# Kernel optimization log

Hardware: AMD Instinct MI355X
Metric: run time of the kernel (lower is better)

Reference implementation:

```python
import jax, jax.numpy as jnp
import numpy as np

N_NODES = 50000
N_EDGES = 500000
D_NODE = 256
D_EDGE = 256
FINAL_OUT = 256
NEG_SLOPE = 0.01  # torch LeakyReLU default


def _linear_params(key, d_in, d_out):
    kw, kb = jax.random.split(key)
    s = 1.0 / np.sqrt(d_in)
    W = jax.random.uniform(kw, (d_in, d_out), jnp.float32, -s, s)
    b = jax.random.uniform(kb, (d_out,), jnp.float32, -s, s)
    return W, b


def setup_inputs() -> dict:
    key = jax.random.key(0)
    ks = jax.random.split(key, 8)
    in1 = D_NODE + D_EDGE          # 512
    hid1 = 2 * in1                 # 1024
    out1 = hid1 // 2               # 512
    in2 = out1 + D_NODE            # 768
    hid2 = 2 * in2                 # 1536
    W1, b1 = _linear_params(ks[0], in1, hid1)
    W2, b2 = _linear_params(ks[1], hid1, out1)
    W3, b3 = _linear_params(ks[2], in2, hid2)
    W4, b4 = _linear_params(ks[3], hid2, FINAL_OUT)
    x = jax.random.normal(ks[4], (N_NODES, D_NODE), jnp.float32)
    edge_attr = jax.random.normal(ks[5], (N_EDGES, D_EDGE), jnp.float32)
    edge_index = jax.random.randint(ks[6], (2, N_EDGES), 0, N_NODES, jnp.int64)
    u = jax.random.normal(ks[7], (1, 16), jnp.float32)
    batch = jnp.zeros((N_NODES,), jnp.int64)
    return {"x": x, "edge_index": edge_index, "edge_attr": edge_attr,
            "u": u, "batch": batch,
            "W1": W1, "b1": b1, "W2": W2, "b2": b2,
            "W3": W3, "b3": b3, "W4": W4, "b4": b4}


def _leaky(v):
    return jnp.where(v >= 0, v, NEG_SLOPE * v)


def reference(x, edge_index, edge_attr, u, batch, W1, b1, W2, b2, W3, b3, W4, b4):
    row, col = edge_index[0], edge_index[1]
    # gather source-node features and concat edge features: [E, D_NODE+D_EDGE]
    m = jnp.concatenate([x[row], edge_attr], axis=1)
    # node_mlp_1
    m = _leaky(m @ W1 + b1) @ W2 + b2            # [E, out1]
    # scatter-mean over destination nodes (count clamped to 1, as torch_scatter)
    agg = jax.ops.segment_sum(m, col, num_segments=x.shape[0])
    cnt = jax.ops.segment_sum(jnp.ones((m.shape[0],), m.dtype), col,
                              num_segments=x.shape[0])
    agg = agg / jnp.maximum(cnt, 1.0)[:, None]   # [N, out1]
    # node_mlp_2
    h = jnp.concatenate([x, agg], axis=1)        # [N, in2]
    return _leaky(h @ W3 + b3) @ W4 + b4         # [N, FINAL_OUT]
```

## Files before the change

### kernel.cpp

```cpp
#include <hip/hip_runtime.h>

typedef __bf16 bf16x8 __attribute__((ext_vector_type(8)));
typedef float fx4 __attribute__((ext_vector_type(4)));
typedef unsigned short u16x8 __attribute__((ext_vector_type(8)));
typedef unsigned short u16x4 __attribute__((ext_vector_type(4)));

__device__ __forceinline__ unsigned short f2b(float f) {
  unsigned u = __float_as_uint(f);
  u = (u + 0x7fffu + ((u >> 16) & 1u)) >> 16;
  return (unsigned short)u;
}
__device__ __forceinline__ float b2f(unsigned short s) {
  return __uint_as_float((unsigned)s << 16);
}

__device__ __forceinline__ void gload16(const void* g, void* l) {
  __builtin_amdgcn_global_load_lds(
      (const __attribute__((address_space(1))) unsigned int*)g,
      (__attribute__((address_space(3))) unsigned int*)l, 16, 0, 0);
}

template<int MODE, int K, int N, int NT, bool EAB>
__global__ __launch_bounds__(256)
void gemm_k(const unsigned short* __restrict__ A,
            const unsigned short* __restrict__ xb,
            const unsigned short* __restrict__ eas,
            const float* __restrict__ eaf,
            const float* __restrict__ aggH_in,
            const float* __restrict__ cnt,
            const unsigned short* __restrict__ agg2b_in,
            const unsigned short* __restrict__ zxb,
            const int* __restrict__ perm,
            const int* __restrict__ ssrc,
            const int* __restrict__ sdst,
            const unsigned short* __restrict__ Bt,
            const float* __restrict__ bias,
            float* __restrict__ outf,
            unsigned short* __restrict__ outb,
            int M, int base, int mt, int mtc)
{
  const int bid = blockIdx.x;
  const int xcd = bid & 7;
  const int sl  = bid >> 3;
  const int tile_n = sl % NT;
  const int tile_m = xcd * mtc + sl / NT;
  if (tile_m >= mt) return;
  const int mbase = tile_m * 128;

  constexpr int SMEM = (MODE == 1) ? 51216 : 16384;
  __shared__ __align__(16) char smem[SMEM];
  unsigned short* Al = (unsigned short*)smem;
  unsigned short* Bl = (unsigned short*)(smem + 8192);

  const int t = threadIdx.x;
  const int w = t >> 6, l = t & 63;
  const int wr = w >> 1, wc = w & 1;
  const int lr = l & 15, lk = l >> 4;

  fx4 zero = {0.f, 0.f, 0.f, 0.f};
  fx4 acc[4][4];
#pragma unroll
  for (int i = 0; i < 4; i++)
#pragma unroll
    for (int j = 0; j < 4; j++) acc[i][j] = zero;

  if constexpr (MODE == 1) {
#pragma unroll
    for (int q = 0; q < 8; ++q) {
      const int c = q * 256 + t;
      const int zrow = c >> 4, zu = c & 15;
      int gr = mbase + zrow; if (gr >= M) gr = M - 1;
      gload16(zxb + (size_t)ssrc[gr] * 1024 + tile_n * 128 + zu * 8,
              (char*)smem + 18448 + c * 16);
    }
  }

  for (int k0 = 0; k0 < K; k0 += 32) {
#pragma unroll
    for (int it = 0; it < 2; ++it) {
      const int c = t + it * 256;
      const int row = c >> 2, u = c & 3;
      gload16(Bt + (size_t)(tile_n * 128 + row) * K + (k0 + u * 8),
              (char*)Bl + c * 16);
      int rl = mbase + row; if (rl >= M) rl = M - 1;
      if constexpr (MODE == 1) {
        if constexpr (EAB) {
          gload16(eas + (size_t)rl * 256 + (k0 + u * 8), (char*)Al + c * 16);
        } else {
          const int e = perm[rl];
          const float* s = eaf + (size_t)e * 256 + (k0 + u * 8);
          fx4 f0 = *(const fx4*)s, f1 = *(const fx4*)(s + 4);
          u16x8 v;
          v[0]=f2b(f0[0]); v[1]=f2b(f0[1]); v[2]=f2b(f0[2]); v[3]=f2b(f0[3]);
          v[4]=f2b(f1[0]); v[5]=f2b(f1[1]); v[6]=f2b(f1[2]); v[7]=f2b(f1[3]);
          *(u16x8*)((char*)Al + c * 16) = v;
        }
      } else if constexpr (MODE == 2) {
        const float ct = cnt[rl];
        const float rs = 1.f / fmaxf(ct, 1.f);
        const float* s = aggH_in + (size_t)rl * 1024 + (k0 + u * 8);
        fx4 f0 = *(const fx4*)s, f1 = *(const fx4*)(s + 4);
        u16x8 v;
        v[0]=f2b(f0[0]*rs); v[1]=f2b(f0[1]*rs); v[2]=f2b(f0[2]*rs); v[3]=f2b(f0[3]*rs);
        v[4]=f2b(f1[0]*rs); v[5]=f2b(f1[1]*rs); v[6]=f2b(f1[2]*rs); v[7]=f2b(f1[3]*rs);
        *(u16x8*)((char*)Al + c * 16) = v;
      } else if constexpr (MODE == 3) {
        const int node = base + rl;
        if (k0 < 256)
          gload16(xb + (size_t)node * 256 + (k0 + u * 8), (char*)Al + c * 16);
        else
          gload16(agg2b_in + (size_t)node * 512 + (k0 - 256) + u * 8,
                  (char*)Al + c * 16);
      } else if constexpr (MODE == 5) {
        gload16(xb + (size_t)rl * 256 + (k0 + u * 8), (char*)Al + c * 16);
      } else {
        gload16(A + (size_t)rl * K + (k0 + u * 8), (char*)Al + c * 16);
      }
    }
    __syncthreads();

    bf16x8 af[4], bfr[4];
    const int mb0 = wr * 64, nb0 = wc * 64;
#pragma unroll
    for (int i = 0; i < 4; i++)
      af[i] = *(const bf16x8*)(Al + (mb0 + i * 16 + lr) * 32 + lk * 8);
#pragma unroll
    for (int j = 0; j < 4; j++)
      bfr[j] = *(const bf16x8*)(Bl + (nb0 + j * 16 + lr) * 32 + lk * 8);
#pragma unroll
    for (int i = 0; i < 4; i++)
#pragma unroll
      for (int j = 0; j < 4; j++)
        acc[i][j] = __builtin_amdgcn_mfma_f32_16x16x32_bf16(af[i], bfr[j],
                                                            acc[i][j], 0, 0, 0);
    __syncthreads();
  }

  if constexpr (MODE == 1) {
    int rows = M - mbase; if (rows > 128) rows = 128;
    unsigned short* CL = (unsigned short*)smem;
    int* runs_s = (int*)(smem + 16896);
    int* runs_e = (int*)(smem + 17408);
    int* runs_d = (int*)(smem + 17920);
    unsigned long long* wmask = (unsigned long long*)(smem + 18432);
    const unsigned short* ZL = (const unsigned short*)(smem + 18448);
    int flag = 0;
    if (t < 128)
      flag = (t < rows) && ((t == 0) || (sdst[mbase + t] != sdst[mbase + t - 1]));
    unsigned long long bm = __ballot(flag);
    if (l == 0 && w < 2) wmask[w] = bm;
    __syncthreads();
    const unsigned long long m0 = wmask[0], m1 = wmask[1];
    const int nruns = __builtin_popcountll(m0) + __builtin_popcountll(m1);
    if (flag) {
      int rank, rend;
      if (t < 64) {
        rank = __builtin_popcountll(m0 & ((t == 0) ? 0ull : ((1ull << t) - 1)));
        unsigned long long above = (t == 63) ? 0ull : (m0 & (~0ull << (t + 1)));
        if (above) rend = __builtin_ctzll(above);
        else if (m1) rend = 64 + __builtin_ctzll(m1);
        else rend = rows;
      } else {
        const int tt = t - 64;
        rank = __builtin_popcountll(m0) +
               __builtin_popcountll(m1 & ((tt == 0) ? 0ull : ((1ull << tt) - 1)));
        unsigned long long above = (tt == 63) ? 0ull : (m1 & (~0ull << (tt + 1)));
        rend = above ? 64 + __builtin_ctzll(above) : rows;
      }
      runs_s[rank] = t; runs_e[rank] = rend; runs_d[rank] = sdst[mbase + t];
    }
    const int lc = wc * 16 + lr;
    const int nn_base = tile_n * 128 + wc * 64 + lr;
    for (int jj = 0; jj < 2; ++jj) {
#pragma unroll
      for (int jp = 0; jp < 2; ++jp) {
        const int j = jj * 2 + jp;
        const float bj = bias[nn_base + j * 16];
        const int cloc = wc * 64 + j * 16 + lr;
#pragma unroll
        for (int i = 0; i < 4; i++)
#pragma unroll
          for (int r = 0; r < 4; r++) {
            const int lrow = wr * 64 + i * 16 + lk * 4 + r;
            float v = acc[i][j][r] + bj + b2f(ZL[lrow * 128 + cloc]);
            v = v >= 0.f ? v : 0.01f * v;
            CL[lrow * 66 + jp * 32 + lc] = f2b(v);
          }
      }
      __syncthreads();
      for (int task = t; task < nruns * 64; task += 256) {
        const int ri = task >> 6, c = task & 63;
        const int rs = runs_s[ri], re = runs_e[ri];
        float s = 0.f;
        for (int r = rs; r < re; ++r) s += b2f(CL[r * 66 + c]);
        const int jp = c >> 5, w16 = (c >> 4) & 1, clr = c & 15;
        const int n = tile_n * 128 + w16 * 64 + (jj * 2 + jp) * 16 + clr;
        float* addr = outf + (size_t)runs_d[ri] * 1024 + n;
        const bool open = (rs == 0 && mbase > 0) || (re == rows && mbase + rows < M);
        if (open) atomicAdd(addr, s); else *addr = s;
      }
      __syncthreads();
    }
  } else {
#pragma unroll
    for (int j = 0; j < 4; j++) {
      const int n = tile_n * 128 + wc * 64 + j * 16 + lr;
      float bj = 0.f;
      if constexpr (MODE == 2 || MODE == 3 || MODE == 4) bj = bias[n];
#pragma unroll
      for (int i = 0; i < 4; i++) {
        const int m0 = mbase + wr * 64 + i * 16 + lk * 4;
#pragma unroll
        for (int r = 0; r < 4; r++) {
          const int m = m0 + r;
          if (m < M) {
            float v = acc[i][j][r];
            if constexpr (MODE == 2) {
              v += (cnt[m] > 0.f ? bj : 0.f);
              outb[(size_t)m * N + n] = f2b(v);
            } else if constexpr (MODE == 3) {
              v += bj;
              v = v >= 0.f ? v : 0.01f * v;
              outb[(size_t)m * N + n] = f2b(v);
            } else if constexpr (MODE == 5) {
              outb[(size_t)m * N + n] = f2b(v);
            } else {
              outf[(size_t)(base + m) * N + n] = v + bj;
            }
          }
        }
      }
    }
  }
}

__global__ void fix_idx_k(const int* __restrict__ src, int* __restrict__ dst, int n2) {
  int i = blockIdx.x * blockDim.x + threadIdx.x;
  if (i >= n2) return;
  bool is64 = true;
#pragma unroll
  for (int p = 0; p < 16; ++p) is64 = is64 && (src[2 * p + 1] == 0);
  dst[i] = is64 ? src[2 * i] : src[i];
}

__global__ void cvt_f2b_k(const float* __restrict__ x, unsigned short* __restrict__ o,
                          long n4) {
  long i = (long)blockIdx.x * blockDim.x + threadIdx.x;
  if (i < n4) {
    fx4 f = *(const fx4*)(x + i * 4);
    u16x4 v; v[0]=f2b(f[0]); v[1]=f2b(f[1]); v[2]=f2b(f[2]); v[3]=f2b(f[3]);
    *(u16x4*)(o + i * 4) = v;
  }
}

__global__ void cvt_eas_k(const float* __restrict__ ea, const int* __restrict__ perm,
                          unsigned short* __restrict__ eas, int E) {
  long i = (long)blockIdx.x * blockDim.x + threadIdx.x;
  if (i >= (long)E * 64) return;
  const int s = (int)(i >> 6), q = (int)(i & 63);
  const float* src = ea + (size_t)perm[s] * 256 + q * 4;
  fx4 f = *(const fx4*)src;
  u16x4 v; v[0]=f2b(f[0]); v[1]=f2b(f[1]); v[2]=f2b(f[2]); v[3]=f2b(f[3]);
  *(u16x4*)(eas + (size_t)s * 256 + q * 4) = v;
}

__global__ void cvt_w_k(const float* __restrict__ W, unsigned short* __restrict__ Wt,
                        int K, int N) {
  long i = (long)blockIdx.x * blockDim.x + threadIdx.x;
  if (i < (long)K * N) {
    int k = (int)(i / N), n = (int)(i % N);
    Wt[(size_t)n * K + k] = f2b(W[i]);
  }
}

__global__ void cnt_kk(const int* __restrict__ ecol, float* __restrict__ cnt, int E) {
  int i = blockIdx.x * blockDim.x + threadIdx.x;
  if (i < E) atomicAdd(cnt + ecol[i], 1.f);
}

__global__ __launch_bounds__(1024)
void scan_k(const float* __restrict__ cnt, int* __restrict__ pos, int Nn) {
  __shared__ int sdata[1024];
  __shared__ int carry;
  if (threadIdx.x == 0) carry = 0;
  __syncthreads();
  for (int bb = 0; bb < Nn; bb += 1024) {
    const int i = bb + threadIdx.x;
    const int v = (i < Nn) ? (int)cnt[i] : 0;
    sdata[threadIdx.x] = v;
    __syncthreads();
    for (int off = 1; off < 1024; off <<= 1) {
      int tv = (threadIdx.x >= off) ? sdata[threadIdx.x - off] : 0;
      __syncthreads();
      sdata[threadIdx.x] += tv;
      __syncthreads();
    }
    const int excl = sdata[threadIdx.x] - v + carry;
    if (i < Nn) pos[i] = excl;
    __syncthreads();
    if (threadIdx.x == 1023) carry += sdata[1023];
    __syncthreads();
  }
}

__global__ void perm_k(const int* __restrict__ idx, int E, int* __restrict__ pos,
                       int* __restrict__ perm, int* __restrict__ ssrc,
                       int* __restrict__ sdst) {
  int e = blockIdx.x * blockDim.x + threadIdx.x;
  if (e >= E) return;
  const int d = idx[E + e];
  const int s = atomicAdd(pos + d, 1);
  perm[s] = e;
  ssrc[s] = idx[e];
  sdst[s] = d;
}

extern "C" void kernel_launch(void* const* d_in, const int* in_sizes, int n_in,
                              void* d_out, int out_size, void* d_ws, size_t ws_size,
                              hipStream_t stream)
{
  const float* x  = (const float*)d_in[0];
  const int* eraw = (const int*)d_in[1];
  const float* ea = (const float*)d_in[2];
  const float* W1 = (const float*)d_in[5];
  const float* b1 = (const float*)d_in[6];
  const float* W2 = (const float*)d_in[7];
  const float* b2 = (const float*)d_in[8];
  const float* W3 = (const float*)d_in[9];
  const float* b3 = (const float*)d_in[10];
  const float* W4 = (const float*)d_in[11];
  const float* b4 = (const float*)d_in[12];
  float* out = (float*)d_out;

  const int Nn = in_sizes[0] / 256;
  const int E  = in_sizes[1] / 2;

  char* p = (char*)d_ws;
  auto take = [&](size_t bytes) -> char* {
    char* r = p; p += (bytes + 255) & ~(size_t)255; return r;
  };
  unsigned short* W1xt = (unsigned short*)take((size_t)1024 * 256 * 2);
  unsigned short* W1et = (unsigned short*)take((size_t)1024 * 256 * 2);
  unsigned short* W2t  = (unsigned short*)take((size_t)1024 * 512 * 2);
  unsigned short* W3t  = (unsigned short*)take((size_t)768 * 1536 * 2);
  unsigned short* W4t  = (unsigned short*)take((size_t)1536 * 256 * 2);
  int* idx  = (int*)take((size_t)2 * E * 4);
  float* cnt  = (float*)take((size_t)Nn * 4);
  float* aggH = (float*)take((size_t)Nn * 1024 * 4);
  size_t zlen = (size_t)(p - (char*)cnt);
  unsigned short* agg2b = (unsigned short*)take((size_t)Nn * 512 * 2);
  unsigned short* xb    = (unsigned short*)take((size_t)Nn * 256 * 2);
  unsigned short* zxb   = (unsigned short*)take((size_t)Nn * 1024 * 2);
  int* pos  = (int*)take((size_t)Nn * 4);
  int* perm = (int*)take((size_t)E * 4);
  int* ssrc = (int*)take((size_t)E * 4);
  int* sdst = (int*)take((size_t)E * 4);

  long avail = (long)ws_size - (long)(p - (char*)d_ws);

  unsigned short* eas = nullptr;
  const long eas_bytes = (((long)E * 256 * 2) + 255) & ~255L;
  if (avail >= eas_bytes + 128 * 3072 + 1024) {
    eas = (unsigned short*)take((size_t)E * 256 * 2);
    avail -= eas_bytes;
  }
  long bandN = avail / 3072;  bandN &= ~127L;
  if (bandN > 50048) bandN = 50048;
  if (bandN < 128)   bandN = 128;
  unsigned short* H3 = (unsigned short*)take((size_t)bandN * 3072);

  hipMemsetAsync(cnt, 0, zlen, stream);
  fix_idx_k<<<(2 * E + 255) / 256, 256, 0, stream>>>(eraw, idx, 2 * E);
  cnt_kk<<<(E + 255) / 256, 256, 0, stream>>>(idx + E, cnt, E);
  scan_k<<<1, 1024, 0, stream>>>(cnt, pos, Nn);
  perm_k<<<(E + 255) / 256, 256, 0, stream>>>(idx, E, pos, perm, ssrc, sdst);
  cvt_f2b_k<<<(Nn * 64 + 255) / 256, 256, 0, stream>>>(x, xb, (long)Nn * 64);
  if (eas)
    cvt_eas_k<<<(int)(((long)E * 64 + 255) / 256), 256, 0, stream>>>(ea, perm,
                                                                     eas, E);
  cvt_w_k<<<(256 * 1024 + 255) / 256, 256, 0, stream>>>(W1, W1xt, 256, 1024);
  cvt_w_k<<<(256 * 1024 + 255) / 256, 256, 0, stream>>>(W1 + 256 * 1024, W1et,
                                                        256, 1024);
  cvt_w_k<<<(1024 * 512 + 255) / 256, 256, 0, stream>>>(W2, W2t, 1024, 512);
  cvt_w_k<<<(768 * 1536 + 255) / 256, 256, 0, stream>>>(W3, W3t, 768, 1536);
  cvt_w_k<<<(1536 * 256 + 255) / 256, 256, 0, stream>>>(W4, W4t, 1536, 256);

  {
    const int mt = (Nn + 127) / 128, mtc = (mt + 7) / 8;
    gemm_k<5, 256, 1024, 8, false><<<mtc * 8 * 8, 256, 0, stream>>>(
        nullptr, xb, nullptr, nullptr, nullptr, nullptr, nullptr, nullptr,
        nullptr, nullptr, nullptr, W1xt, nullptr, nullptr, zxb, Nn, 0, mt, mtc);
  }

  {
    const int mt = (E + 127) / 128, mtc = (mt + 7) / 8;
    const int grid = mtc * 8 * 8;
    if (eas)
      gemm_k<1, 256, 1024, 8, true><<<grid, 256, 0, stream>>>(
          nullptr, nullptr, eas, ea, nullptr, nullptr, nullptr, zxb, perm,
          ssrc, sdst, W1et, b1, aggH, nullptr, E, 0, mt, mtc);
    else
      gemm_k<1, 256, 1024, 8, false><<<grid, 256, 0, stream>>>(
          nullptr, nullptr, nullptr, ea, nullptr, nullptr, nullptr, zxb, perm,
          ssrc, sdst, W1et, b1, aggH, nullptr, E, 0, mt, mtc);
  }

  {
    const int mt = (Nn + 127) / 128, mtc = (mt + 7) / 8;
    gemm_k<2, 1024, 512, 4, false><<<mtc * 8 * 4, 256, 0, stream>>>(
        nullptr, nullptr, nullptr, nullptr, aggH, cnt, nullptr, nullptr,
        nullptr, nullptr, nullptr, W2t, b2, nullptr, agg2b, Nn, 0, mt, mtc);
  }

  for (long base = 0; base < Nn; base += bandN) {
    long rem = Nn - base;
    int mb = (int)(rem < bandN ? rem : bandN);
    int mt = (mb + 127) / 128, mtc = (mt + 7) / 8;
    gemm_k<3, 768, 1536, 12, false><<<mtc * 8 * 12, 256, 0, stream>>>(
        nullptr, xb, nullptr, nullptr, nullptr, nullptr, agg2b, nullptr,
        nullptr, nullptr, nullptr, W3t, b3, nullptr, H3, mb, (int)base, mt, mtc);
    gemm_k<4, 1536, 256, 2, false><<<mtc * 8 * 2, 256, 0, stream>>>(
        H3, nullptr, nullptr, nullptr, nullptr, nullptr, nullptr, nullptr,
        nullptr, nullptr, nullptr, W4t, b4, out, nullptr, mb, (int)base, mt, mtc);
  }
}
```

Before: 1.645 ms.

## Double-buffer LDS tiles in non-edge GEMM modes to overlap loads with MFMA

Refactors the K-loop into stage and compute lambdas. For all modes except the edge GEMM, LDS is doubled so the next K-slice is fetched into the alternate buffer while MFMAs run on the current one, which drops one barrier per iteration. The edge mode keeps single buffering because its LDS is already large. The cost is doubled shared memory for those modes, which may lower occupancy.

```diff
diff --git a/kernel.cpp b/kernel.cpp
--- a/kernel.cpp
+++ b/kernel.cpp
@@ -47,10 +47,8 @@
   if (tile_m >= mt) return;
   const int mbase = tile_m * 128;
 
-  constexpr int SMEM = (MODE == 1) ? 51216 : 16384;
+  constexpr int SMEM = (MODE == 1) ? 51216 : 32768;
   __shared__ __align__(16) char smem[SMEM];
-  unsigned short* Al = (unsigned short*)smem;
-  unsigned short* Bl = (unsigned short*)(smem + 8192);
 
   const int t = threadIdx.x;
   const int w = t >> 6, l = t & 63;
@@ -64,28 +62,20 @@
 #pragma unroll
     for (int j = 0; j < 4; j++) acc[i][j] = zero;
 
-  if constexpr (MODE == 1) {
-#pragma unroll
-    for (int q = 0; q < 8; ++q) {
-      const int c = q * 256 + t;
-      const int zrow = c >> 4, zu = c & 15;
-      int gr = mbase + zrow; if (gr >= M) gr = M - 1;
-      gload16(zxb + (size_t)ssrc[gr] * 1024 + tile_n * 128 + zu * 8,
-              (char*)smem + 18448 + c * 16);
-    }
-  }
-
-  for (int k0 = 0; k0 < K; k0 += 32) {
+  auto STAGE = [&](int ks, int b) {
+    const int k0 = ks * 32;
+    char* Ab = (char*)smem + b * 16384;
+    char* Bb = Ab + 8192;
 #pragma unroll
     for (int it = 0; it < 2; ++it) {
       const int c = t + it * 256;
       const int row = c >> 2, u = c & 3;
       gload16(Bt + (size_t)(tile_n * 128 + row) * K + (k0 + u * 8),
-              (char*)Bl + c * 16);
+              Bb + c * 16);
       int rl = mbase + row; if (rl >= M) rl = M - 1;
       if constexpr (MODE == 1) {
         if constexpr (EAB) {
-          gload16(eas + (size_t)rl * 256 + (k0 + u * 8), (char*)Al + c * 16);
+          gload16(eas + (size_t)rl * 256 + (k0 + u * 8), Ab + c * 16);
         } else {
           const int e = perm[rl];
           const float* s = eaf + (size_t)e * 256 + (k0 + u * 8);
@@ -93,7 +83,7 @@
           u16x8 v;
           v[0]=f2b(f0[0]); v[1]=f2b(f0[1]); v[2]=f2b(f0[2]); v[3]=f2b(f0[3]);
           v[4]=f2b(f1[0]); v[5]=f2b(f1[1]); v[6]=f2b(f1[2]); v[7]=f2b(f1[3]);
-          *(u16x8*)((char*)Al + c * 16) = v;
+          *(u16x8*)(Ab + c * 16) = v;
         }
       } else if constexpr (MODE == 2) {
         const float ct = cnt[rl];
@@ -103,22 +93,25 @@
         u16x8 v;
         v[0]=f2b(f0[0]*rs); v[1]=f2b(f0[1]*rs); v[2]=f2b(f0[2]*rs); v[3]=f2b(f0[3]*rs);
         v[4]=f2b(f1[0]*rs); v[5]=f2b(f1[1]*rs); v[6]=f2b(f1[2]*rs); v[7]=f2b(f1[3]*rs);
-        *(u16x8*)((char*)Al + c * 16) = v;
+        *(u16x8*)(Ab + c * 16) = v;
       } else if constexpr (MODE == 3) {
         const int node = base + rl;
         if (k0 < 256)
-          gload16(xb + (size_t)node * 256 + (k0 + u * 8), (char*)Al + c * 16);
+          gload16(xb + (size_t)node * 256 + (k0 + u * 8), Ab + c * 16);
         else
           gload16(agg2b_in + (size_t)node * 512 + (k0 - 256) + u * 8,
-                  (char*)Al + c * 16);
+                  Ab + c * 16);
       } else if constexpr (MODE == 5) {
-        gload16(xb + (size_t)rl * 256 + (k0 + u * 8), (char*)Al + c * 16);
+        gload16(xb + (size_t)rl * 256 + (k0 + u * 8), Ab + c * 16);
       } else {
-        gload16(A + (size_t)rl * K + (k0 + u * 8), (char*)Al + c * 16);
+        gload16(A + (size_t)rl * K + (k0 + u * 8), Ab + c * 16);
       }
     }
-    __syncthreads();
-
+  };
+
+  auto COMPUTE = [&](int b) {
+    const unsigned short* Al = (const unsigned short*)((char*)smem + b * 16384);
+    const unsigned short* Bl = Al + 4096;
     bf16x8 af[4], bfr[4];
     const int mb0 = wr * 64, nb0 = wc * 64;
 #pragma unroll
@@ -133,7 +126,33 @@
       for (int j = 0; j < 4; j++)
         acc[i][j] = __builtin_amdgcn_mfma_f32_16x16x32_bf16(af[i], bfr[j],
                                                             acc[i][j], 0, 0, 0);
+  };
+
+  const int NK = K / 32;
+  if constexpr (MODE == 1) {
+#pragma unroll
+    for (int q = 0; q < 8; ++q) {
+      const int c = q * 256 + t;
+      const int zrow = c >> 4, zu = c & 15;
+      int gr = mbase + zrow; if (gr >= M) gr = M - 1;
+      gload16(zxb + (size_t)ssrc[gr] * 1024 + tile_n * 128 + zu * 8,
+              (char*)smem + 18448 + c * 16);
+    }
+    for (int ks = 0; ks < NK; ++ks) {
+      STAGE(ks, 0);
+      __syncthreads();
+      COMPUTE(0);
+      __syncthreads();
+    }
+  } else {
+    STAGE(0, 0);
     __syncthreads();
+    for (int ks = 0; ks < NK; ++ks) {
+      const int cur = ks & 1;
+      if (ks + 1 < NK) STAGE(ks + 1, cur ^ 1);
+      COMPUTE(cur);
+      __syncthreads();
+    }
   }
 
   if constexpr (MODE == 1) {
```

Measured after the change: 1.645 ms. About the same (+0.0%).
